# Kernel optimization log

Hardware: AMD Instinct MI355X
Metric: run time of the kernel (lower is better)

Reference implementation:

```python
import jax, jax.numpy as jnp
import numpy as np
import math

S, B, D = 2048, 2, 1024
H = 16
DH = D // H
WIN = 256
DIL = 1


def setup_inputs() -> dict:
    key = jax.random.key(0)
    ks = jax.random.split(key, 10)
    std = 1.0 / math.sqrt(D)
    return {
        "x": jax.random.normal(ks[0], (S, B, D), jnp.float32),
        "beta": jax.random.normal(ks[1], (H,), jnp.float32) * 0.02,
        "Wq": jax.random.normal(ks[2], (D, D), jnp.float32) * std,
        "bq": jnp.zeros((D,), jnp.float32),
        "Wk": jax.random.normal(ks[3], (D, D), jnp.float32) * std,
        "bk": jnp.zeros((D,), jnp.float32),
        "Wv": jax.random.normal(ks[4], (D, D), jnp.float32) * std,
        "bv": jnp.zeros((D,), jnp.float32),
        "Wo": jax.random.normal(ks[5], (D, D), jnp.float32) * std,
        "bo": jnp.zeros((D,), jnp.float32),
    }


def _split_heads(t):
    # (S, B, D) -> (B*H, S, DH), matching rearrange 's b (h d) -> (b h) s d'
    return t.reshape(S, B, H, DH).transpose(1, 2, 0, 3).reshape(B * H, S, DH)


def reference(x, beta, Wq, bq, Wk, bk, Wv, bv, Wo, bo):
    q = _split_heads(x @ Wq + bq)
    k = _split_heads(x @ Wk + bk)
    v = _split_heads(x @ Wv + bv)

    # per-head learnable temperature: q / (sqrt(d_head) * exp(beta))
    beta_exp = jnp.tile(jnp.exp(beta), B)  # (B*H,), head index = z % H
    q = q / (jnp.sqrt(jnp.asarray(DH, x.dtype)) * beta_exp)[:, None, None]

    # causal dilated windowed mask
    idx = jnp.arange(S)
    diff = idx[:, None] - idx[None, :]
    allowed = (diff >= 0) & (diff <= DIL * (WIN - 1)) & (diff % DIL == 0)
    mask = jnp.where(allowed, jnp.asarray(0.0, x.dtype), jnp.asarray(-jnp.inf, x.dtype))

    scores = jnp.einsum('zqd,zkd->zqk', q, k) + mask[None]
    # attention sink: extra zero-logit column absorbing probability mass
    scores = jnp.concatenate([scores, jnp.zeros((B * H, S, 1), scores.dtype)], axis=-1)
    attn = jax.nn.softmax(scores, axis=-1)[..., :-1]

    out = jnp.einsum('zqk,zkd->zqd', attn, v)
    # (B*H, S, DH) -> (S, B, D)
    out = out.reshape(B, H, S, DH).transpose(2, 0, 1, 3).reshape(S, B, D)
    return out @ Wo + bo
```

## Files before the change

### kernel.cpp

```cpp
#include <hip/hip_runtime.h>
#include <math.h>

#define S_LEN  2048
#define BATCH  2
#define DM     1024
#define NHEAD  16
#define DHEAD  64
#define WIN    256
#define MROWS  4096

#define PPAD 68

#define BM 256
#define BN 192
#define BK 64

#define OM 128
#define ON 64

typedef __attribute__((ext_vector_type(8))) short bf16x8;
typedef __attribute__((ext_vector_type(4))) float f32x4;

__device__ __forceinline__ unsigned short f2b(float f) {
    unsigned int u = __float_as_uint(f);
    return (unsigned short)((u + 0x7fffu + ((u >> 16) & 1u)) >> 16);
}
__device__ __forceinline__ void gld16(const void* g, void* l) {
    __builtin_amdgcn_global_load_lds(
        (const __attribute__((address_space(1))) void*)g,
        (__attribute__((address_space(3))) void*)l, 16, 0, 0);
}
__device__ __forceinline__ bf16x8 pack8(float4 a, float4 b) {
    bf16x8 r;
    r[0] = (short)f2b(a.x); r[1] = (short)f2b(a.y);
    r[2] = (short)f2b(a.z); r[3] = (short)f2b(a.w);
    r[4] = (short)f2b(b.x); r[5] = (short)f2b(b.y);
    r[6] = (short)f2b(b.z); r[7] = (short)f2b(b.w);
    return r;
}

__global__ __launch_bounds__(256)
void cvtx(const float* __restrict__ x, unsigned short* __restrict__ xb)
{
    const int i = (blockIdx.x * 256 + threadIdx.x) * 4;
    float4 f = *(const float4*)(x + i);
    ushort4 o; o.x = f2b(f.x); o.y = f2b(f.y); o.z = f2b(f.z); o.w = f2b(f.w);
    *(ushort4*)(xb + i) = o;
}

__global__ __launch_bounds__(256)
void twcvt4(const float* __restrict__ W0, const float* __restrict__ W1,
            const float* __restrict__ W2, const float* __restrict__ W3,
            unsigned short* __restrict__ T0, unsigned short* __restrict__ T1,
            unsigned short* __restrict__ T2, unsigned short* __restrict__ T3)
{
    const int zz = blockIdx.z;
    const float* W = (zz == 0) ? W0 : (zz == 1) ? W1 : (zz == 2) ? W2 : W3;
    unsigned short* WT = (zz == 0) ? T0 : (zz == 1) ? T1 : (zz == 2) ? T2 : T3;

    __shared__ float t32[32][33];
    const int bx = blockIdx.x * 32;
    const int by = blockIdx.y * 32;
    const int c  = threadIdx.x & 31;
    const int r0 = threadIdx.x >> 5;
#pragma unroll
    for (int p = 0; p < 4; ++p)
        t32[r0 + 8 * p][c] = W[(size_t)(by + r0 + 8 * p) * DM + bx + c];
    __syncthreads();
#pragma unroll
    for (int p = 0; p < 4; ++p)
        WT[(size_t)(bx + r0 + 8 * p) * DM + by + c] = f2b(t32[c][r0 + 8 * p]);
}

__global__ __launch_bounds__(512, 2)
void gemm_qkv(const unsigned short* __restrict__ A,
              const unsigned short* __restrict__ BT,
              const float* __restrict__ b0,
              const float* __restrict__ b1,
              const float* __restrict__ b2,
              const float* __restrict__ beta,
              unsigned short* __restrict__ Cb)
{
    __shared__ unsigned short Ab[2][BM * BK];
    __shared__ unsigned short Bb[2][BN * BK];

    const int t   = threadIdx.x;
    const int ln  = t & 63;
    const int wv  = t >> 6;
    const int wr  = wv & 3;
    const int wc  = wv >> 2;
    const int m16 = ln & 15;
    const int g   = ln >> 4;
    const int sw  = m16 & 7;

    const int rowBase = blockIdx.y * BM;
    const int colBase = blockIdx.x * BN;

    const int sr  = t >> 3;
    const int scx = (t & 7) ^ (sr & 7);
    const size_t gOff = (size_t)sr * DM + scx * 8;
    const int    ldOff = t * 8;

    f32x4 acc[4][6];
#pragma unroll
    for (int u = 0; u < 4; ++u)
#pragma unroll
        for (int v = 0; v < 6; ++v)
            acc[u][v] = (f32x4){0.f, 0.f, 0.f, 0.f};

    {
        const unsigned short* a0 = A  + (size_t)rowBase * DM + gOff;
        const unsigned short* bt = BT + (size_t)colBase * DM + gOff;
#pragma unroll
        for (int cb = 0; cb < 3; ++cb)
            gld16(bt + (size_t)cb * 64 * DM, &Bb[0][cb * 4096 + ldOff]);
#pragma unroll
        for (int ca = 0; ca < 4; ++ca)
            gld16(a0 + (size_t)ca * 64 * DM, &Ab[0][ca * 4096 + ldOff]);
        asm volatile("s_waitcnt vmcnt(0)" ::: "memory");
        __builtin_amdgcn_s_barrier();
        __builtin_amdgcn_sched_barrier(0);
    }

    for (int kt = 0; kt < DM / BK; ++kt) {
        const int cur = kt & 1;
        const unsigned short* Ac = Ab[cur];
        const unsigned short* Bc = Bb[cur];
        unsigned short* An = Ab[cur ^ 1];
        unsigned short* Bn = Bb[cur ^ 1];
        const bool hn = (kt < DM / BK - 1);
        const unsigned short* aS = A  + (size_t)rowBase * DM + (kt + 1) * BK + gOff;
        const unsigned short* bS = BT + (size_t)colBase * DM + (kt + 1) * BK + gOff;

        bf16x8 af0[4], bf0[6];
#pragma unroll
        for (int u = 0; u < 4; ++u)
            af0[u] = *(const bf16x8*)&Ac[(wr * 64 + u * 16 + m16) * BK + ((g ^ sw) * 8)];
#pragma unroll
        for (int v = 0; v < 6; ++v)
            bf0[v] = *(const bf16x8*)&Bc[(wc * 96 + v * 16 + m16) * BK + ((g ^ sw) * 8)];

        if (hn) {
            gld16(bS,                    &Bn[ldOff]);
            gld16(bS + (size_t)64 * DM,  &Bn[4096 + ldOff]);
            gld16(bS + (size_t)128 * DM, &Bn[2 * 4096 + ldOff]);
            gld16(aS,                    &An[ldOff]);
            gld16(aS + (size_t)64 * DM,  &An[4096 + ldOff]);
            gld16(aS + (size_t)128 * DM, &An[2 * 4096 + ldOff]);
            gld16(aS + (size_t)192 * DM, &An[3 * 4096 + ldOff]);
        }

        __builtin_amdgcn_s_setprio(1);
#pragma unroll
        for (int u = 0; u < 4; ++u)
#pragma unroll
            for (int v = 0; v < 6; ++v)
                acc[u][v] = __builtin_amdgcn_mfma_f32_16x16x32_bf16(
                    af0[u], bf0[v], acc[u][v], 0, 0, 0);
        __builtin_amdgcn_s_setprio(0);

        bf16x8 af1[4], bf1[6];
#pragma unroll
        for (int u = 0; u < 4; ++u)
            af1[u] = *(const bf16x8*)&Ac[(wr * 64 + u * 16 + m16) * BK + (((4 | g) ^ sw) * 8)];
#pragma unroll
        for (int v = 0; v < 6; ++v)
            bf1[v] = *(const bf16x8*)&Bc[(wc * 96 + v * 16 + m16) * BK + (((4 | g) ^ sw) * 8)];

        __builtin_amdgcn_s_setprio(1);
#pragma unroll
        for (int u = 0; u < 4; ++u)
#pragma unroll
            for (int v = 0; v < 6; ++v)
                acc[u][v] = __builtin_amdgcn_mfma_f32_16x16x32_bf16(
                    af1[u], bf1[v], acc[u][v], 0, 0, 0);
        __builtin_amdgcn_s_setprio(0);

        if (hn)
            asm volatile("s_waitcnt vmcnt(0)" ::: "memory");
        __builtin_amdgcn_s_barrier();
        __builtin_amdgcn_sched_barrier(0);
    }

    const int q4 = g * 4;
#pragma unroll
    for (int v = 0; v < 6; ++v) {
        const int col = colBase + wc * 96 + v * 16 + m16;
        const int sec = col >> 10;
        const int h   = (col >> 6) & (NHEAD - 1);
        const int dh  = col & 63;
        if (sec < 2) {
            const float bi = (sec == 0 ? b0 : b1)[col & (DM - 1)];
            const float sc = (sec == 0) ? 0.125f * __expf(-beta[h]) : 1.0f;
            unsigned short* base = Cb + (size_t)sec * MROWS * DM;
#pragma unroll
            for (int u = 0; u < 4; ++u)
#pragma unroll
                for (int r = 0; r < 4; ++r) {
                    const int row = rowBase + wr * 64 + u * 16 + q4 + r;
                    const int s = row >> 1, bb = row & 1;
                    const int z = bb * NHEAD + h;
                    base[((size_t)z * S_LEN + s) * DHEAD + dh] =
                        f2b((acc[u][v][r] + bi) * sc);
                }
        } else {
            unsigned short* vtb = Cb + (size_t)2 * MROWS * DM;
            const float bi = b2[col & (DM - 1)];
#pragma unroll
            for (int u = 0; u < 4; ++u) {
                const int row0 = rowBase + wr * 64 + u * 16 + q4;
                const int s0   = row0 >> 1;
                ushort2 p0, p1;
                p0.x = f2b(acc[u][v][0] + bi);
                p0.y = f2b(acc[u][v][2] + bi);
                p1.x = f2b(acc[u][v][1] + bi);
                p1.y = f2b(acc[u][v][3] + bi);
                *(ushort2*)(vtb + ((size_t)(h * DHEAD + dh) * S_LEN + s0)) = p0;
                *(ushort2*)(vtb + ((size_t)((NHEAD + h) * DHEAD + dh) * S_LEN + s0)) = p1;
            }
        }
    }
}

__global__ __launch_bounds__(256, 2)
void gemm_out(const unsigned short* __restrict__ A,
              const unsigned short* __restrict__ BT,
              const float* __restrict__ bias,
              float* __restrict__ Cf)
{
    __shared__ unsigned short As[2][OM * BK];
    __shared__ unsigned short Bs[2][ON * BK];

    const int t  = threadIdx.x;
    const int wv = t >> 6, ln = t & 63;
    const int wr = wv >> 1, wc = wv & 1;
    const int m16 = ln & 15, g = ln >> 4;
    const int sw  = m16 & 7;

    const int rowBase = blockIdx.y * OM;
    const int colBase = blockIdx.x * ON;

    const int sr  = t >> 3;
    const int scx = (t & 7) ^ (sr & 7);
    const size_t gOff = (size_t)sr * DM + scx * 8;
    const int    ldOff = t * 8;

    f32x4 acc[4][2];
#pragma unroll
    for (int u = 0; u < 4; ++u)
#pragma unroll
        for (int v = 0; v < 2; ++v)
            acc[u][v] = (f32x4){0.f, 0.f, 0.f, 0.f};

    {
        const unsigned short* a0 = A  + (size_t)rowBase * DM + gOff;
        const unsigned short* bt = BT + (size_t)colBase * DM + gOff;
#pragma unroll
        for (int j = 0; j < 4; ++j)
            gld16(a0 + (size_t)(j * 32) * DM, &As[0][j * 2048 + ldOff]);
#pragma unroll
        for (int j = 0; j < 2; ++j)
            gld16(bt + (size_t)(j * 32) * DM, &Bs[0][j * 2048 + ldOff]);
        asm volatile("s_waitcnt vmcnt(0)" ::: "memory");
        __builtin_amdgcn_s_barrier();
        __builtin_amdgcn_sched_barrier(0);
    }

    for (int kt = 0; kt < DM / BK; ++kt) {
        const int cur = kt & 1;
        const unsigned short* Ac = As[cur];
        const unsigned short* Bc = Bs[cur];
        unsigned short* An = As[cur ^ 1];
        unsigned short* Bn = Bs[cur ^ 1];
        const bool hn = (kt < DM / BK - 1);
        const unsigned short* aS = A  + (size_t)rowBase * DM + (kt + 1) * BK + gOff;
        const unsigned short* bS = BT + (size_t)colBase * DM + (kt + 1) * BK + gOff;

        bf16x8 af0[4], bf0[2];
#pragma unroll
        for (int u = 0; u < 4; ++u)
            af0[u] = *(const bf16x8*)&Ac[(wr * 64 + u * 16 + m16) * BK + ((g ^ sw) * 8)];
#pragma unroll
        for (int v = 0; v < 2; ++v)
            bf0[v] = *(const bf16x8*)&Bc[(wc * 32 + v * 16 + m16) * BK + ((g ^ sw) * 8)];

        if (hn) {
#pragma unroll
            for (int j = 0; j < 4; ++j)
                gld16(aS + (size_t)(j * 32) * DM, &An[j * 2048 + ldOff]);
#pragma unroll
            for (int j = 0; j < 2; ++j)
                gld16(bS + (size_t)(j * 32) * DM, &Bn[j * 2048 + ldOff]);
        }

        __builtin_amdgcn_s_setprio(1);
#pragma unroll
        for (int u = 0; u < 4; ++u)
#pragma unroll
            for (int v = 0; v < 2; ++v)
                acc[u][v] = __builtin_amdgcn_mfma_f32_16x16x32_bf16(
                    af0[u], bf0[v], acc[u][v], 0, 0, 0);
        __builtin_amdgcn_s_setprio(0);

        bf16x8 af1[4], bf1[2];
#pragma unroll
        for (int u = 0; u < 4; ++u)
            af1[u] = *(const bf16x8*)&Ac[(wr * 64 + u * 16 + m16) * BK + (((4 | g) ^ sw) * 8)];
#pragma unroll
        for (int v = 0; v < 2; ++v)
            bf1[v] = *(const bf16x8*)&Bc[(wc * 32 + v * 16 + m16) * BK + (((4 | g) ^ sw) * 8)];

        __builtin_amdgcn_s_setprio(1);
#pragma unroll
        for (int u = 0; u < 4; ++u)
#pragma unroll
            for (int v = 0; v < 2; ++v)
                acc[u][v] = __builtin_amdgcn_mfma_f32_16x16x32_bf16(
                    af1[u], bf1[v], acc[u][v], 0, 0, 0);
        __builtin_amdgcn_s_setprio(0);

        if (hn)
            asm volatile("s_waitcnt vmcnt(0)" ::: "memory");
        __builtin_amdgcn_s_barrier();
        __builtin_amdgcn_sched_barrier(0);
    }

    const int q4 = g * 4;
#pragma unroll
    for (int v = 0; v < 2; ++v) {
        const int col = colBase + wc * 32 + v * 16 + m16;
        const float bi = bias[col];
#pragma unroll
        for (int u = 0; u < 4; ++u)
#pragma unroll
            for (int r = 0; r < 4; ++r) {
                const int row = rowBase + wr * 64 + u * 16 + q4 + r;
                Cf[(size_t)row * DM + col] = acc[u][v][r] + bi;
            }
    }
}

__global__ __launch_bounds__(256, 3)
void attn_mfma(const unsigned short* __restrict__ q,
               const unsigned short* __restrict__ k,
               const unsigned short* __restrict__ vt,
               unsigned short* __restrict__ ao)
{
    __shared__ unsigned short Ks[2][64 * 64];
    __shared__ unsigned short Vs[2][64 * 64];
    __shared__ float Ps[64][PPAD];

    const int t   = threadIdx.x;
    const int wv  = t >> 6, ln = t & 63;
    const int m16 = ln & 15, g = ln >> 4;
    const int sw  = m16 & 7;
    const int z   = blockIdx.y;
    const int q0  = blockIdx.x * 64;
    const size_t zbase = (size_t)z * S_LEN * DHEAD;

    const int sr  = t >> 3;
    const int scx = (t & 7) ^ (sr & 7);
    const unsigned short* kS = k  + zbase + (size_t)sr * DHEAD + scx * 8;
    const unsigned short* vS = vt + ((size_t)z * DHEAD + sr) * S_LEN + scx * 8;
    const int ldOff = t * 8;

    const unsigned short* qrow = q + zbase + (size_t)(q0 + wv * 16 + m16) * DHEAD;
    bf16x8 qf0 = *(const bf16x8*)(qrow + g * 8);
    bf16x8 qf1 = *(const bf16x8*)(qrow + 32 + g * 8);

    f32x4 oacc[4];
#pragma unroll
    for (int v4 = 0; v4 < 4; ++v4) oacc[v4] = (f32x4){0.f, 0.f, 0.f, 0.f};
    float lr[4];
#pragma unroll
    for (int r = 0; r < 4; ++r) lr[r] = 1.f;

    const int c0 = (blockIdx.x < 4) ? (4 - (int)blockIdx.x) : 0;

    {
        const int kb = q0 - 256 + c0 * 64;
        gld16(kS + (size_t)kb * DHEAD,        &Ks[0][ldOff]);
        gld16(kS + (size_t)(kb + 32) * DHEAD, &Ks[0][2048 + ldOff]);
        gld16(vS + kb,                        &Vs[0][ldOff]);
        gld16(vS + (size_t)32 * S_LEN + kb,   &Vs[0][2048 + ldOff]);
        asm volatile("s_waitcnt vmcnt(0)" ::: "memory");
        __builtin_amdgcn_s_barrier();
        __builtin_amdgcn_sched_barrier(0);
    }

    for (int c = c0; c < 5; ++c) {
        const int cur = (c - c0) & 1;
        const int kb  = q0 - 256 + c * 64;
        const bool hn = (c < 4);

        if (hn) {
            const int kn = kb + 64;
            gld16(kS + (size_t)kn * DHEAD,        &Ks[cur ^ 1][ldOff]);
            gld16(kS + (size_t)(kn + 32) * DHEAD, &Ks[cur ^ 1][2048 + ldOff]);
            gld16(vS + kn,                        &Vs[cur ^ 1][ldOff]);
            gld16(vS + (size_t)32 * S_LEN + kn,   &Vs[cur ^ 1][2048 + ldOff]);
        }

        f32x4 sacc[4];
#pragma unroll
        for (int v4 = 0; v4 < 4; ++v4) {
            sacc[v4] = (f32x4){0.f, 0.f, 0.f, 0.f};
            bf16x8 kf0 = *(const bf16x8*)&Ks[cur][(v4 * 16 + m16) * 64 + ((g ^ sw) * 8)];
            sacc[v4] = __builtin_amdgcn_mfma_f32_16x16x32_bf16(qf0, kf0, sacc[v4], 0, 0, 0);
            bf16x8 kf1 = *(const bf16x8*)&Ks[cur][(v4 * 16 + m16) * 64 + (((4 | g) ^ sw) * 8)];
            sacc[v4] = __builtin_amdgcn_mfma_f32_16x16x32_bf16(qf1, kf1, sacc[v4], 0, 0, 0);
        }

        const bool mhi = (c == 4), mlo = (c == 0);
#pragma unroll
        for (int r = 0; r < 4; ++r) {
            const int ig = q0 + wv * 16 + g * 4 + r;
            float rsum = 0.f;
#pragma unroll
            for (int v4 = 0; v4 < 4; ++v4) {
                const int jg = kb + v4 * 16 + m16;
                float x = sacc[v4][r];
                const bool valid = (!mhi || jg <= ig) && (!mlo || jg >= ig - (WIN - 1));
                x = valid ? x : -1e30f;
                const float pp = __expf(x);
                Ps[wv * 16 + g * 4 + r][v4 * 16 + m16] = pp;
                rsum += pp;
            }
#pragma unroll
            for (int off = 1; off < 16; off <<= 1)
                rsum += __shfl_xor(rsum, off, 64);
            lr[r] += rsum;
        }

        asm volatile("s_waitcnt lgkmcnt(0)" ::: "memory");
        __builtin_amdgcn_sched_barrier(0);

        const float* prow = &Ps[wv * 16 + m16][0];
        bf16x8 pf0 = pack8(*(const float4*)(prow + g * 8),
                           *(const float4*)(prow + g * 8 + 4));
        bf16x8 pf1 = pack8(*(const float4*)(prow + 32 + g * 8),
                           *(const float4*)(prow + 32 + g * 8 + 4));
#pragma unroll
        for (int v4 = 0; v4 < 4; ++v4) {
            bf16x8 vf0 = *(const bf16x8*)&Vs[cur][(v4 * 16 + m16) * 64 + ((g ^ sw) * 8)];
            oacc[v4] = __builtin_amdgcn_mfma_f32_16x16x32_bf16(pf0, vf0, oacc[v4], 0, 0, 0);
            bf16x8 vf1 = *(const bf16x8*)&Vs[cur][(v4 * 16 + m16) * 64 + (((4 | g) ^ sw) * 8)];
            oacc[v4] = __builtin_amdgcn_mfma_f32_16x16x32_bf16(pf1, vf1, oacc[v4], 0, 0, 0);
        }

        if (hn) {
            asm volatile("s_waitcnt vmcnt(0)" ::: "memory");
            __builtin_amdgcn_s_barrier();
            __builtin_amdgcn_sched_barrier(0);
        }
    }

    const int bb = z >> 4, h = z & 15;
#pragma unroll
    for (int r = 0; r < 4; ++r) {
        const int ig  = q0 + wv * 16 + g * 4 + r;
        const float inv = 1.f / lr[r];
#pragma unroll
        for (int v4 = 0; v4 < 4; ++v4)
            ao[(size_t)(ig * BATCH + bb) * DM + h * DHEAD + v4 * 16 + m16] =
                f2b(oacc[v4][r] * inv);
    }
}

extern "C" void kernel_launch(void* const* d_in, const int* in_sizes, int n_in,
                              void* d_out, int out_size, void* d_ws, size_t ws_size,
                              hipStream_t stream)
{
    const float* x    = (const float*)d_in[0];
    const float* beta = (const float*)d_in[1];
    const float* Wq   = (const float*)d_in[2];
    const float* bq   = (const float*)d_in[3];
    const float* Wk   = (const float*)d_in[4];
    const float* bk   = (const float*)d_in[5];
    const float* Wv   = (const float*)d_in[6];
    const float* bv   = (const float*)d_in[7];
    const float* Wo   = (const float*)d_in[8];
    const float* bo   = (const float*)d_in[9];
    float* out = (float*)d_out;

    unsigned short* w = (unsigned short*)d_ws;
    const size_t seg = (size_t)MROWS * DM;
    unsigned short* qb  = w;
    unsigned short* kb  = w + seg;
    unsigned short* vtb = w + 2 * seg;
    unsigned short* ab  = w + 3 * seg;
    unsigned short* xb  = w + 4 * seg;
    unsigned short* wtq = w + 5 * seg;
    unsigned short* wtk = wtq + (size_t)DM * DM;
    unsigned short* wtv = wtk + (size_t)DM * DM;
    unsigned short* wto = wtv + (size_t)DM * DM;

    cvtx<<<4096, 256, 0, stream>>>(x, xb);
    twcvt4<<<dim3(32, 32, 4), 256, 0, stream>>>(Wq, Wk, Wv, Wo, wtq, wtk, wtv, wto);

    gemm_qkv<<<dim3(3072 / BN, MROWS / BM), 512, 0, stream>>>(
        xb, wtq, bq, bk, bv, beta, qb);

    attn_mfma<<<dim3(S_LEN / 64, BATCH * NHEAD), 256, 0, stream>>>(qb, kb, vtb, ab);

    gemm_out<<<dim3(DM / ON, MROWS / OM), 256, 0, stream>>>(ab, wto, bo, out);
}
```

Baseline: 170.5 us.

## Deepen QKV GEMM pipeline to prefetch two tiles ahead with interleaved quadrant MFMAs

```diff
diff --git a/kernel.cpp b/kernel.cpp
--- a/kernel.cpp
+++ b/kernel.cpp
@@ -14,6 +14,7 @@
 #define BM 256
 #define BN 192
 #define BK 64
+#define NKT (DM / BK)
 
 #define OM 128
 #define ON 64
@@ -81,7 +82,7 @@
               const float* __restrict__ beta,
               unsigned short* __restrict__ Cb)
 {
-    __shared__ unsigned short Ab[2][BM * BK];
+    __shared__ unsigned short Ab[3][BM * BK];
     __shared__ unsigned short Bb[2][BN * BK];
 
     const int t   = threadIdx.x;
@@ -108,75 +109,138 @@
         for (int v = 0; v < 6; ++v)
             acc[u][v] = (f32x4){0.f, 0.f, 0.f, 0.f};
 
+    const unsigned short* aBase = A  + (size_t)rowBase * DM + gOff;
+    const unsigned short* bBase = BT + (size_t)colBase * DM + gOff;
+
     {
-        const unsigned short* a0 = A  + (size_t)rowBase * DM + gOff;
-        const unsigned short* bt = BT + (size_t)colBase * DM + gOff;
+#pragma unroll
+        for (int ca = 0; ca < 4; ++ca)
+            gld16(aBase + (size_t)ca * 64 * DM, &Ab[0][ca * 4096 + ldOff]);
 #pragma unroll
         for (int cb = 0; cb < 3; ++cb)
-            gld16(bt + (size_t)cb * 64 * DM, &Bb[0][cb * 4096 + ldOff]);
+            gld16(bBase + (size_t)cb * 64 * DM, &Bb[0][cb * 4096 + ldOff]);
 #pragma unroll
         for (int ca = 0; ca < 4; ++ca)
-            gld16(a0 + (size_t)ca * 64 * DM, &Ab[0][ca * 4096 + ldOff]);
-        asm volatile("s_waitcnt vmcnt(0)" ::: "memory");
-        __builtin_amdgcn_s_barrier();
-        __builtin_amdgcn_sched_barrier(0);
-    }
-
-    for (int kt = 0; kt < DM / BK; ++kt) {
-        const int cur = kt & 1;
-        const unsigned short* Ac = Ab[cur];
-        const unsigned short* Bc = Bb[cur];
-        unsigned short* An = Ab[cur ^ 1];
-        unsigned short* Bn = Bb[cur ^ 1];
-        const bool hn = (kt < DM / BK - 1);
-        const unsigned short* aS = A  + (size_t)rowBase * DM + (kt + 1) * BK + gOff;
-        const unsigned short* bS = BT + (size_t)colBase * DM + (kt + 1) * BK + gOff;
-
-        bf16x8 af0[4], bf0[6];
-#pragma unroll
-        for (int u = 0; u < 4; ++u)
-            af0[u] = *(const bf16x8*)&Ac[(wr * 64 + u * 16 + m16) * BK + ((g ^ sw) * 8)];
-#pragma unroll
-        for (int v = 0; v < 6; ++v)
-            bf0[v] = *(const bf16x8*)&Bc[(wc * 96 + v * 16 + m16) * BK + ((g ^ sw) * 8)];
-
-        if (hn) {
-            gld16(bS,                    &Bn[ldOff]);
-            gld16(bS + (size_t)64 * DM,  &Bn[4096 + ldOff]);
-            gld16(bS + (size_t)128 * DM, &Bn[2 * 4096 + ldOff]);
-            gld16(aS,                    &An[ldOff]);
-            gld16(aS + (size_t)64 * DM,  &An[4096 + ldOff]);
-            gld16(aS + (size_t)128 * DM, &An[2 * 4096 + ldOff]);
-            gld16(aS + (size_t)192 * DM, &An[3 * 4096 + ldOff]);
-        }
-
+            gld16(aBase + BK + (size_t)ca * 64 * DM, &Ab[1][ca * 4096 + ldOff]);
+#pragma unroll
+        for (int cb = 0; cb < 3; ++cb)
+            gld16(bBase + BK + (size_t)cb * 64 * DM, &Bb[1][cb * 4096 + ldOff]);
+        asm volatile("s_waitcnt vmcnt(7)" ::: "memory");
+        __builtin_amdgcn_s_barrier();
+        __builtin_amdgcn_sched_barrier(0);
+    }
+
+    bf16x8 afr[4][2], bfr[6][2];
+
+    for (int kt = 0; kt < NKT; ++kt) {
+        const unsigned short* Ac = Ab[kt % 3];
+        const unsigned short* Bc = Bb[kt & 1];
+        unsigned short* An2 = Ab[(kt + 2) % 3];
+        unsigned short* Bn2 = Bb[kt & 1];
+        const bool h2 = (kt < NKT - 2);
+        const unsigned short* aS = aBase + (size_t)(kt + 2) * BK;
+        const unsigned short* bS = bBase + (size_t)(kt + 2) * BK;
+
+#pragma unroll
+        for (int u = 0; u < 2; ++u) {
+            const int ro = (wr * 64 + u * 16 + m16) * BK;
+            afr[u][0] = *(const bf16x8*)&Ac[ro + ((g ^ sw) * 8)];
+            afr[u][1] = *(const bf16x8*)&Ac[ro + (((4 | g) ^ sw) * 8)];
+        }
+#pragma unroll
+        for (int v = 0; v < 3; ++v) {
+            const int ro = (wc * 96 + v * 16 + m16) * BK;
+            bfr[v][0] = *(const bf16x8*)&Bc[ro + ((g ^ sw) * 8)];
+            bfr[v][1] = *(const bf16x8*)&Bc[ro + (((4 | g) ^ sw) * 8)];
+        }
+        if (h2) {
+            gld16(aS,                   &An2[ldOff]);
+            gld16(aS + (size_t)64 * DM, &An2[4096 + ldOff]);
+        }
+        __builtin_amdgcn_s_barrier();
+        __builtin_amdgcn_sched_barrier(0);
         __builtin_amdgcn_s_setprio(1);
 #pragma unroll
-        for (int u = 0; u < 4; ++u)
-#pragma unroll
-            for (int v = 0; v < 6; ++v)
-                acc[u][v] = __builtin_amdgcn_mfma_f32_16x16x32_bf16(
-                    af0[u], bf0[v], acc[u][v], 0, 0, 0);
+        for (int u = 0; u < 2; ++u)
+#pragma unroll
+            for (int v = 0; v < 3; ++v) {
+                acc[u][v] = __builtin_amdgcn_mfma_f32_16x16x32_bf16(
+                    afr[u][0], bfr[v][0], acc[u][v], 0, 0, 0);
+                acc[u][v] = __builtin_amdgcn_mfma_f32_16x16x32_bf16(
+                    afr[u][1], bfr[v][1], acc[u][v], 0, 0, 0);
+            }
         __builtin_amdgcn_s_setprio(0);
-
-        bf16x8 af1[4], bf1[6];
-#pragma unroll
-        for (int u = 0; u < 4; ++u)
-            af1[u] = *(const bf16x8*)&Ac[(wr * 64 + u * 16 + m16) * BK + (((4 | g) ^ sw) * 8)];
-#pragma unroll
-        for (int v = 0; v < 6; ++v)
-            bf1[v] = *(const bf16x8*)&Bc[(wc * 96 + v * 16 + m16) * BK + (((4 | g) ^ sw) * 8)];
-
+        __builtin_amdgcn_s_barrier();
+        __builtin_amdgcn_sched_barrier(0);
+
+#pragma unroll
+        for (int v = 3; v < 6; ++v) {
+            const int ro = (wc * 96 + v * 16 + m16) * BK;
+            bfr[v][0] = *(const bf16x8*)&Bc[ro + ((g ^ sw) * 8)];
+            bfr[v][1] = *(const bf16x8*)&Bc[ro + (((4 | g) ^ sw) * 8)];
+        }
+        if (h2) {
+            gld16(aS + (size_t)128 * DM, &An2[2 * 4096 + ldOff]);
+            gld16(aS + (size_t)192 * DM, &An2[3 * 4096 + ldOff]);
+        }
+        __builtin_amdgcn_s_barrier();
+        __builtin_amdgcn_sched_barrier(0);
         __builtin_amdgcn_s_setprio(1);
 #pragma unroll
-        for (int u = 0; u < 4; ++u)
-#pragma unroll
-            for (int v = 0; v < 6; ++v)
-                acc[u][v] = __builtin_amdgcn_mfma_f32_16x16x32_bf16(
-                    af1[u], bf1[v], acc[u][v], 0, 0, 0);
+        for (int u = 0; u < 2; ++u)
+#pragma unroll
+            for (int v = 3; v < 6; ++v) {
+                acc[u][v] = __builtin_amdgcn_mfma_f32_16x16x32_bf16(
+                    afr[u][0], bfr[v][0], acc[u][v], 0, 0, 0);
+                acc[u][v] = __builtin_amdgcn_mfma_f32_16x16x32_bf16(
+                    afr[u][1], bfr[v][1], acc[u][v], 0, 0, 0);
+            }
         __builtin_amdgcn_s_setprio(0);
-
-        if (hn)
+        __builtin_amdgcn_s_barrier();
+        __builtin_amdgcn_sched_barrier(0);
+
+#pragma unroll
+        for (int u = 2; u < 4; ++u) {
+            const int ro = (wr * 64 + u * 16 + m16) * BK;
+            afr[u][0] = *(const bf16x8*)&Ac[ro + ((g ^ sw) * 8)];
+            afr[u][1] = *(const bf16x8*)&Ac[ro + (((4 | g) ^ sw) * 8)];
+        }
+        if (h2) {
+            gld16(bS,                   &Bn2[ldOff]);
+            gld16(bS + (size_t)64 * DM, &Bn2[4096 + ldOff]);
+        }
+        __builtin_amdgcn_s_barrier();
+        __builtin_amdgcn_sched_barrier(0);
+        __builtin_amdgcn_s_setprio(1);
+#pragma unroll
+        for (int u = 2; u < 4; ++u)
+#pragma unroll
+            for (int v = 0; v < 3; ++v) {
+                acc[u][v] = __builtin_amdgcn_mfma_f32_16x16x32_bf16(
+                    afr[u][0], bfr[v][0], acc[u][v], 0, 0, 0);
+                acc[u][v] = __builtin_amdgcn_mfma_f32_16x16x32_bf16(
+                    afr[u][1], bfr[v][1], acc[u][v], 0, 0, 0);
+            }
+        __builtin_amdgcn_s_setprio(0);
+        __builtin_amdgcn_s_barrier();
+        __builtin_amdgcn_sched_barrier(0);
+
+        if (h2)
+            gld16(bS + (size_t)128 * DM, &Bn2[2 * 4096 + ldOff]);
+        __builtin_amdgcn_s_setprio(1);
+#pragma unroll
+        for (int u = 2; u < 4; ++u)
+#pragma unroll
+            for (int v = 3; v < 6; ++v) {
+                acc[u][v] = __builtin_amdgcn_mfma_f32_16x16x32_bf16(
+                    afr[u][0], bfr[v][0], acc[u][v], 0, 0, 0);
+                acc[u][v] = __builtin_amdgcn_mfma_f32_16x16x32_bf16(
+                    afr[u][1], bfr[v][1], acc[u][v], 0, 0, 0);
+            }
+        __builtin_amdgcn_s_setprio(0);
+        if (kt < NKT - 2)
+            asm volatile("s_waitcnt vmcnt(7)" ::: "memory");
+        else if (kt == NKT - 2)
             asm volatile("s_waitcnt vmcnt(0)" ::: "memory");
         __builtin_amdgcn_s_barrier();
         __builtin_amdgcn_sched_barrier(0);
@@ -305,10 +369,10 @@
         bf16x8 af1[4], bf1[2];
 #pragma unroll
         for (int u = 0; u < 4; ++u)
-            af1[u] = *(const bf16x8*)&Ac[(wr * 64 + u * 16 + m16) * BK + (((4 | g) ^ sw) * 8)];
+            af1[u] = *(const bf16x8*)&As[cur][(wr * 64 + u * 16 + m16) * BK + (((4 | g) ^ sw) * 8)];
 #pragma unroll
         for (int v = 0; v < 2; ++v)
-            bf1[v] = *(const bf16x8*)&Bc[(wc * 32 + v * 16 + m16) * BK + (((4 | g) ^ sw) * 8)];
+            bf1[v] = *(const bf16x8*)&Bs[cur][(wc * 32 + v * 16 + m16) * BK + (((4 | g) ^ sw) * 8)];
 
         __builtin_amdgcn_s_setprio(1);
 #pragma unroll
```

Measured after the change: 173.2 us. About the same (+1.6%).
